# Performance work log

Measured on AMD Instinct MI355X. Metric: run time of the kernel, lower is better.

Reference implementation:

```python
import jax, jax.numpy as jnp
import numpy as np

DECAY = 0.9      # decay_rate l
LR = 0.5         # fast-weight learning_rate e
STEP = 3         # inner-loop iterations
EPS = 1e-3       # keras LayerNormalization default epsilon

B, D_IN, U = 128, 256, 512


def setup_inputs() -> dict:
    key = jax.random.key(0)
    ks = jax.random.split(key, 6)
    return {
        "inputs": jax.random.normal(ks[0], (B, D_IN), dtype=jnp.float32),
        "prev_state": jax.random.normal(ks[1], (B, U), dtype=jnp.float32),
        "A": jax.random.normal(ks[2], (B, U, U), dtype=jnp.float32) * 0.01,
        "C": jax.random.normal(ks[3], (D_IN, U), dtype=jnp.float32) * (1.0 / np.sqrt(D_IN)),
        # original: glorot-identity init scaled by 0.05; randomized here, same math
        "W_h": jax.random.normal(ks[4], (U, U), dtype=jnp.float32) * 0.05,
        "bias": jax.random.normal(ks[5], (U,), dtype=jnp.float32) * 0.01,
        "gamma": jnp.ones((U,), dtype=jnp.float32),
        "beta": jnp.zeros((U,), dtype=jnp.float32),
    }


def _layer_norm(x, gamma, beta):
    m = jnp.mean(x, axis=-1, keepdims=True)
    v = jnp.var(x, axis=-1, keepdims=True)
    return (x - m) * jax.lax.rsqrt(v + EPS) * gamma + beta


def reference(inputs, prev_state, A, C, W_h, bias, gamma, beta):
    # slow path: h = act(prev @ W_h + x @ C + b)   -> [B, U]
    pre = prev_state @ W_h + inputs @ C
    h = jnp.tanh(pre + bias)
    # fast-weight update: A' = l*A + e * outer(h, h)  -> [B, U, U]
    A_new = DECAY * A + LR * jnp.einsum("bi,bj->bij", h, h)
    # inner loop: h_s = LN(act(prelim + h_s @ A'))  with h_s: [B, 1, U]
    prelim = pre[:, None, :]          # no bias / no activation, matching source
    h_s = h[:, None, :]
    for _ in range(STEP):
        h_s = jnp.tanh(prelim + jnp.einsum("bku,buv->bkv", h_s, A_new))
        h_s = _layer_norm(h_s, gamma, beta)
    out = h_s[:, 0, :]                # [B, U]; also the new recurrent state
    return out, A_new
```

## Files before the change

### kernel.cpp

```cpp
#include <hip/hip_runtime.h>
#include <math.h>

#define UDIM 512
#define DIN  256
#define BATCH 128
#define EPSV 1e-3f

#define NRSEG 8
#define RPB   64
#define HALFR 32

typedef float f4 __attribute__((ext_vector_type(4)));

__global__ __launch_bounds__(256) void k_pre(
    const float* __restrict__ inputs, const float* __restrict__ prev,
    const float* __restrict__ C, const float* __restrict__ Wh,
    const float* __restrict__ bias, float* __restrict__ pre, float* __restrict__ h)
{
    const int b = blockIdx.x >> 1;
    const int v = ((blockIdx.x & 1) << 8) + threadIdx.x;

    __shared__ float sprev[UDIM];
    __shared__ float sinp[DIN];
    for (int i = threadIdx.x; i < UDIM; i += 256) sprev[i] = prev[b * UDIM + i];
    sinp[threadIdx.x] = inputs[b * DIN + threadIdx.x];
    __syncthreads();

    float acc = 0.f;
#pragma unroll 8
    for (int u = 0; u < UDIM; ++u) acc = fmaf(sprev[u], Wh[u * UDIM + v], acc);
#pragma unroll 8
    for (int i = 0; i < DIN; ++i)  acc = fmaf(sinp[i], C[i * UDIM + v], acc);

    pre[b * UDIM + v] = acc;
    h[b * UDIM + v]   = tanhf(acc + bias[v]);
}

__global__ __launch_bounds__(256) void k_mv0(
    const float* __restrict__ A, const float* __restrict__ h,
    float* __restrict__ Anew, float* __restrict__ ypart)
{
    const int bc   = blockIdx.x;
    const int b    = bc >> 3;
    const int rs   = bc & 7;
    const int t    = threadIdx.x;
    const int vg   = t & 127;
    const int col  = vg << 2;
    const int half = t >> 7;

    __shared__ __align__(16) float sh[UDIM];
    __shared__ __align__(16) float spart[2][UDIM];

    sh[t]       = h[(size_t)b * UDIM + t];
    sh[t + 256] = h[(size_t)b * UDIM + t + 256];
    __syncthreads();

    const f4 hv4 = *(const f4*)(sh + col);
    const int row0 = rs * RPB + half * HALFR;
    const float* __restrict__ Ab  = A    + ((size_t)b * UDIM + row0) * UDIM + col;
    float*       __restrict__ Anb = Anew + ((size_t)b * UDIM + row0) * UDIM + col;

    f4 acc = {0.f, 0.f, 0.f, 0.f};
#pragma unroll 8
    for (int k = 0; k < HALFR; ++k) {
        const f4 a4 = __builtin_nontemporal_load((const f4*)(Ab + (size_t)k * UDIM));
        const float hu = sh[row0 + k];
        const float s = 0.5f * hu;
        f4 an;
        an.x = fmaf(s, hv4.x, 0.9f * a4.x);
        an.y = fmaf(s, hv4.y, 0.9f * a4.y);
        an.z = fmaf(s, hv4.z, 0.9f * a4.z);
        an.w = fmaf(s, hv4.w, 0.9f * a4.w);
        *(f4*)(Anb + (size_t)k * UDIM) = an;
        acc.x = fmaf(hu, an.x, acc.x);
        acc.y = fmaf(hu, an.y, acc.y);
        acc.z = fmaf(hu, an.z, acc.z);
        acc.w = fmaf(hu, an.w, acc.w);
    }
    *(f4*)(&spart[half][col]) = acc;
    __syncthreads();

    {
        const float y0 = spart[0][t]       + spart[1][t];
        const float y1 = spart[0][t + 256] + spart[1][t + 256];
        ypart[(size_t)bc * UDIM + t]       = y0;
        ypart[(size_t)bc * UDIM + t + 256] = y1;
    }
}

__global__ __launch_bounds__(256) void k_mv(
    const float* __restrict__ An, const float* __restrict__ pre,
    const float* __restrict__ ypin, const float* __restrict__ gamma,
    const float* __restrict__ beta, float* __restrict__ ypout)
{
    const int bc   = blockIdx.x;
    const int b    = bc >> 3;
    const int rs   = bc & 7;
    const int t    = threadIdx.x;
    const int lane = t & 63;
    const int wave = t >> 6;
    const int vg   = t & 127;
    const int col  = vg << 2;
    const int half = t >> 7;

    __shared__ __align__(16) float sx[UDIM];
    __shared__ float shs[UDIM];
    __shared__ __align__(16) float spart[2][UDIM];
    __shared__ float sred[8];
    __shared__ float sbc[2];

    {
        float y0 = 0.f, y1 = 0.f;
#pragma unroll
        for (int s = 0; s < NRSEG; ++s) {
            y0 += ypin[((size_t)b * NRSEG + s) * UDIM + t];
            y1 += ypin[((size_t)b * NRSEG + s) * UDIM + t + 256];
        }
        const float hs0 = tanhf(pre[(size_t)b * UDIM + t] + y0);
        const float hs1 = tanhf(pre[(size_t)b * UDIM + t + 256] + y1);
        shs[t] = hs0; shs[t + 256] = hs1;
        float s1 = hs0 + hs1, s2 = hs0 * hs0 + hs1 * hs1;
#pragma unroll
        for (int off = 32; off; off >>= 1) {
            s1 += __shfl_xor(s1, off, 64);
            s2 += __shfl_xor(s2, off, 64);
        }
        if (lane == 0) { sred[wave] = s1; sred[4 + wave] = s2; }
    }
    __syncthreads();
    if (t == 0) {
        float m = sred[0] + sred[1] + sred[2] + sred[3];
        float q = sred[4] + sred[5] + sred[6] + sred[7];
        m *= (1.f / UDIM);
        q = q * (1.f / UDIM) - m * m;
        sbc[0] = m;
        sbc[1] = rsqrtf(q + EPSV);
    }
    __syncthreads();
    {
        const float m = sbc[0], r = sbc[1];
        sx[t]       = (shs[t]       - m) * r * gamma[t]       + beta[t];
        sx[t + 256] = (shs[t + 256] - m) * r * gamma[t + 256] + beta[t + 256];
    }
    __syncthreads();

    const int row0 = rs * RPB + half * HALFR;
    const float* __restrict__ Ab = An + ((size_t)b * UDIM + row0) * UDIM + col;

    f4 acc = {0.f, 0.f, 0.f, 0.f};
#pragma unroll 8
    for (int k = 0; k < HALFR; ++k) {
        const f4 a4 = *(const f4*)(Ab + (size_t)k * UDIM);
        const float xu = sx[row0 + k];
        acc.x = fmaf(xu, a4.x, acc.x);
        acc.y = fmaf(xu, a4.y, acc.y);
        acc.z = fmaf(xu, a4.z, acc.z);
        acc.w = fmaf(xu, a4.w, acc.w);
    }
    *(f4*)(&spart[half][col]) = acc;
    __syncthreads();

    {
        const float y0 = spart[0][t]       + spart[1][t];
        const float y1 = spart[0][t + 256] + spart[1][t + 256];
        ypout[(size_t)bc * UDIM + t]       = y0;
        ypout[(size_t)bc * UDIM + t + 256] = y1;
    }
}

__global__ __launch_bounds__(512) void k_fin(
    const float* __restrict__ pre, const float* __restrict__ ypin,
    const float* __restrict__ gamma, const float* __restrict__ beta,
    float* __restrict__ out)
{
    const int b    = blockIdx.x;
    const int t    = threadIdx.x;
    const int lane = t & 63;
    const int wave = t >> 6;

    __shared__ float sred[16];
    __shared__ float sbc[2];

    float y = 0.f;
#pragma unroll
    for (int s = 0; s < NRSEG; ++s) y += ypin[((size_t)b * NRSEG + s) * UDIM + t];
    const float hs = tanhf(pre[(size_t)b * UDIM + t] + y);

    float s1 = hs, s2 = hs * hs;
#pragma unroll
    for (int off = 32; off; off >>= 1) {
        s1 += __shfl_xor(s1, off, 64);
        s2 += __shfl_xor(s2, off, 64);
    }
    if (lane == 0) { sred[wave] = s1; sred[8 + wave] = s2; }
    __syncthreads();
    if (t == 0) {
        float m = 0.f, q = 0.f;
#pragma unroll
        for (int i = 0; i < 8; ++i) { m += sred[i]; q += sred[8 + i]; }
        m *= (1.f / UDIM);
        q = q * (1.f / UDIM) - m * m;
        sbc[0] = m;
        sbc[1] = rsqrtf(q + EPSV);
    }
    __syncthreads();
    out[(size_t)b * UDIM + t] = (hs - sbc[0]) * sbc[1] * gamma[t] + beta[t];
}

extern "C" void kernel_launch(void* const* d_in, const int* in_sizes, int n_in,
                              void* d_out, int out_size, void* d_ws, size_t ws_size,
                              hipStream_t stream) {
    const float* inputs = (const float*)d_in[0];
    const float* prev   = (const float*)d_in[1];
    const float* A      = (const float*)d_in[2];
    const float* C      = (const float*)d_in[3];
    const float* Wh     = (const float*)d_in[4];
    const float* bias   = (const float*)d_in[5];
    const float* gamma  = (const float*)d_in[6];
    const float* beta   = (const float*)d_in[7];

    float* out  = (float*)d_out;
    float* Anew = out + (size_t)BATCH * UDIM;

    float* pre  = (float*)d_ws;
    float* h    = pre  + (size_t)BATCH * UDIM;
    float* ypA  = h    + (size_t)BATCH * UDIM;
    float* ypB  = ypA  + (size_t)BATCH * NRSEG * UDIM;

    k_pre<<<BATCH * 2, 256, 0, stream>>>(inputs, prev, C, Wh, bias, pre, h);
    k_mv0<<<BATCH * NRSEG, 256, 0, stream>>>(A, h, Anew, ypA);
    k_mv <<<BATCH * NRSEG, 256, 0, stream>>>(Anew, pre, ypA, gamma, beta, ypB);
    k_mv <<<BATCH * NRSEG, 256, 0, stream>>>(Anew, pre, ypB, gamma, beta, ypA);
    k_fin<<<BATCH, 512, 0, stream>>>(pre, ypA, gamma, beta, out);
}
```

Before: 132.7 us.

## Use rank-1 identity to read original A and split Anew writes across passes

Rewrites x·A' as 0.9·(x·A) + 0.5·(x·h)·h, so every mat-vec pass reads the original A and adds a cheap dot-product correction instead of reading the freshly written Anew. The first pass now only reads A. The Anew write is split so each of the two later passes writes half the rows, using nontemporal stores. The aim is to spread and overlap the write traffic and avoid a write-then-read dependency, at the cost of extra dot-product reductions and small workspace buffers.

```diff
diff --git a/kernel.cpp b/kernel.cpp
--- a/kernel.cpp
+++ b/kernel.cpp
@@ -36,62 +36,9 @@
     h[b * UDIM + v]   = tanhf(acc + bias[v]);
 }
 
-__global__ __launch_bounds__(256) void k_mv0(
+__global__ __launch_bounds__(256) void k_mv0ro(
     const float* __restrict__ A, const float* __restrict__ h,
-    float* __restrict__ Anew, float* __restrict__ ypart)
-{
-    const int bc   = blockIdx.x;
-    const int b    = bc >> 3;
-    const int rs   = bc & 7;
-    const int t    = threadIdx.x;
-    const int vg   = t & 127;
-    const int col  = vg << 2;
-    const int half = t >> 7;
-
-    __shared__ __align__(16) float sh[UDIM];
-    __shared__ __align__(16) float spart[2][UDIM];
-
-    sh[t]       = h[(size_t)b * UDIM + t];
-    sh[t + 256] = h[(size_t)b * UDIM + t + 256];
-    __syncthreads();
-
-    const f4 hv4 = *(const f4*)(sh + col);
-    const int row0 = rs * RPB + half * HALFR;
-    const float* __restrict__ Ab  = A    + ((size_t)b * UDIM + row0) * UDIM + col;
-    float*       __restrict__ Anb = Anew + ((size_t)b * UDIM + row0) * UDIM + col;
-
-    f4 acc = {0.f, 0.f, 0.f, 0.f};
-#pragma unroll 8
-    for (int k = 0; k < HALFR; ++k) {
-        const f4 a4 = __builtin_nontemporal_load((const f4*)(Ab + (size_t)k * UDIM));
-        const float hu = sh[row0 + k];
-        const float s = 0.5f * hu;
-        f4 an;
-        an.x = fmaf(s, hv4.x, 0.9f * a4.x);
-        an.y = fmaf(s, hv4.y, 0.9f * a4.y);
-        an.z = fmaf(s, hv4.z, 0.9f * a4.z);
-        an.w = fmaf(s, hv4.w, 0.9f * a4.w);
-        *(f4*)(Anb + (size_t)k * UDIM) = an;
-        acc.x = fmaf(hu, an.x, acc.x);
-        acc.y = fmaf(hu, an.y, acc.y);
-        acc.z = fmaf(hu, an.z, acc.z);
-        acc.w = fmaf(hu, an.w, acc.w);
-    }
-    *(f4*)(&spart[half][col]) = acc;
-    __syncthreads();
-
-    {
-        const float y0 = spart[0][t]       + spart[1][t];
-        const float y1 = spart[0][t + 256] + spart[1][t + 256];
-        ypart[(size_t)bc * UDIM + t]       = y0;
-        ypart[(size_t)bc * UDIM + t + 256] = y1;
-    }
-}
-
-__global__ __launch_bounds__(256) void k_mv(
-    const float* __restrict__ An, const float* __restrict__ pre,
-    const float* __restrict__ ypin, const float* __restrict__ gamma,
-    const float* __restrict__ beta, float* __restrict__ ypout)
+    float* __restrict__ ypart, float* __restrict__ dotout)
 {
     const int bc   = blockIdx.x;
     const int b    = bc >> 3;
@@ -103,11 +50,72 @@
     const int col  = vg << 2;
     const int half = t >> 7;
 
+    __shared__ __align__(16) float sh[UDIM];
+    __shared__ __align__(16) float spart[2][UDIM];
+    __shared__ float sred[4];
+
+    sh[t]       = h[(size_t)b * UDIM + t];
+    sh[t + 256] = h[(size_t)b * UDIM + t + 256];
+    __syncthreads();
+
+    float dp = sh[t] * sh[t] + sh[t + 256] * sh[t + 256];
+#pragma unroll
+    for (int off = 32; off; off >>= 1) dp += __shfl_xor(dp, off, 64);
+    if (lane == 0) sred[wave] = dp;
+
+    const int row0 = rs * RPB + half * HALFR;
+    const float* __restrict__ Ab = A + ((size_t)b * UDIM + row0) * UDIM + col;
+
+    f4 acc = {0.f, 0.f, 0.f, 0.f};
+#pragma unroll 8
+    for (int k = 0; k < HALFR; ++k) {
+        const f4 a4 = *(const f4*)(Ab + (size_t)k * UDIM);
+        const float hu = sh[row0 + k];
+        acc.x = fmaf(hu, a4.x, acc.x);
+        acc.y = fmaf(hu, a4.y, acc.y);
+        acc.z = fmaf(hu, a4.z, acc.z);
+        acc.w = fmaf(hu, a4.w, acc.w);
+    }
+    *(f4*)(&spart[half][col]) = acc;
+    __syncthreads();
+
+    {
+        const float y0 = spart[0][t]       + spart[1][t];
+        const float y1 = spart[0][t + 256] + spart[1][t + 256];
+        ypart[(size_t)bc * UDIM + t]       = y0;
+        ypart[(size_t)bc * UDIM + t + 256] = y1;
+    }
+    if (rs == 0 && t == 0)
+        dotout[b] = sred[0] + sred[1] + sred[2] + sred[3];
+}
+
+__global__ __launch_bounds__(256) void k_mv(
+    const float* __restrict__ A, float* __restrict__ Anew,
+    const float* __restrict__ pre, const float* __restrict__ h,
+    const float* __restrict__ ypin, const float* __restrict__ dotin,
+    const float* __restrict__ gamma, const float* __restrict__ beta,
+    float* __restrict__ ypout, float* __restrict__ dotout, const int wh)
+{
+    const int bc   = blockIdx.x;
+    const int b    = bc >> 3;
+    const int rs   = bc & 7;
+    const int t    = threadIdx.x;
+    const int lane = t & 63;
+    const int wave = t >> 6;
+    const int vg   = t & 127;
+    const int col  = vg << 2;
+    const int half = t >> 7;
+
+    __shared__ __align__(16) float sh[UDIM];
     __shared__ __align__(16) float sx[UDIM];
     __shared__ float shs[UDIM];
     __shared__ __align__(16) float spart[2][UDIM];
     __shared__ float sred[8];
+    __shared__ float sred2[4];
     __shared__ float sbc[2];
+
+    sh[t]       = h[(size_t)b * UDIM + t];
+    sh[t + 256] = h[(size_t)b * UDIM + t + 256];
 
     {
         float y0 = 0.f, y1 = 0.f;
@@ -116,6 +124,9 @@
             y0 += ypin[((size_t)b * NRSEG + s) * UDIM + t];
             y1 += ypin[((size_t)b * NRSEG + s) * UDIM + t + 256];
         }
+        const float d = 0.5f * dotin[b];
+        y0 = fmaf(0.9f, y0, d * sh[t]);
+        y1 = fmaf(0.9f, y1, d * sh[t + 256]);
         const float hs0 = tanhf(pre[(size_t)b * UDIM + t] + y0);
         const float hs1 = tanhf(pre[(size_t)b * UDIM + t + 256] + y1);
         shs[t] = hs0; shs[t + 256] = hs1;
@@ -144,18 +155,46 @@
     }
     __syncthreads();
 
+    {
+        float dp = sx[t] * sh[t] + sx[t + 256] * sh[t + 256];
+#pragma unroll
+        for (int off = 32; off; off >>= 1) dp += __shfl_xor(dp, off, 64);
+        if (lane == 0) sred2[wave] = dp;
+    }
+
     const int row0 = rs * RPB + half * HALFR;
-    const float* __restrict__ Ab = An + ((size_t)b * UDIM + row0) * UDIM + col;
+    const float* __restrict__ Ab  = A    + ((size_t)b * UDIM + row0) * UDIM + col;
+    float*       __restrict__ Anb = Anew + ((size_t)b * UDIM + row0) * UDIM + col;
+    const f4 hv4 = *(const f4*)(sh + col);
 
     f4 acc = {0.f, 0.f, 0.f, 0.f};
-#pragma unroll 8
-    for (int k = 0; k < HALFR; ++k) {
-        const f4 a4 = *(const f4*)(Ab + (size_t)k * UDIM);
-        const float xu = sx[row0 + k];
-        acc.x = fmaf(xu, a4.x, acc.x);
-        acc.y = fmaf(xu, a4.y, acc.y);
-        acc.z = fmaf(xu, a4.z, acc.z);
-        acc.w = fmaf(xu, a4.w, acc.w);
+    if (half == wh) {
+#pragma unroll 8
+        for (int k = 0; k < HALFR; ++k) {
+            const f4 a4 = *(const f4*)(Ab + (size_t)k * UDIM);
+            const float xu = sx[row0 + k];
+            const float s  = 0.5f * sh[row0 + k];
+            f4 an;
+            an.x = fmaf(s, hv4.x, 0.9f * a4.x);
+            an.y = fmaf(s, hv4.y, 0.9f * a4.y);
+            an.z = fmaf(s, hv4.z, 0.9f * a4.z);
+            an.w = fmaf(s, hv4.w, 0.9f * a4.w);
+            __builtin_nontemporal_store(an, (f4*)(Anb + (size_t)k * UDIM));
+            acc.x = fmaf(xu, a4.x, acc.x);
+            acc.y = fmaf(xu, a4.y, acc.y);
+            acc.z = fmaf(xu, a4.z, acc.z);
+            acc.w = fmaf(xu, a4.w, acc.w);
+        }
+    } else {
+#pragma unroll 8
+        for (int k = 0; k < HALFR; ++k) {
+            const f4 a4 = *(const f4*)(Ab + (size_t)k * UDIM);
+            const float xu = sx[row0 + k];
+            acc.x = fmaf(xu, a4.x, acc.x);
+            acc.y = fmaf(xu, a4.y, acc.y);
+            acc.z = fmaf(xu, a4.z, acc.z);
+            acc.w = fmaf(xu, a4.w, acc.w);
+        }
     }
     *(f4*)(&spart[half][col]) = acc;
     __syncthreads();
@@ -166,10 +205,13 @@
         ypout[(size_t)bc * UDIM + t]       = y0;
         ypout[(size_t)bc * UDIM + t + 256] = y1;
     }
+    if (rs == 0 && t == 0)
+        dotout[b] = sred2[0] + sred2[1] + sred2[2] + sred2[3];
 }
 
 __global__ __launch_bounds__(512) void k_fin(
-    const float* __restrict__ pre, const float* __restrict__ ypin,
+    const float* __restrict__ pre, const float* __restrict__ h,
+    const float* __restrict__ ypin, const float* __restrict__ dotin,
     const float* __restrict__ gamma, const float* __restrict__ beta,
     float* __restrict__ out)
 {
@@ -184,6 +226,7 @@
     float y = 0.f;
 #pragma unroll
     for (int s = 0; s < NRSEG; ++s) y += ypin[((size_t)b * NRSEG + s) * UDIM + t];
+    y = fmaf(0.9f, y, 0.5f * dotin[b] * h[(size_t)b * UDIM + t]);
     const float hs = tanhf(pre[(size_t)b * UDIM + t] + y);
 
     float s1 = hs, s2 = hs * hs;
@@ -226,10 +269,15 @@
     float* h    = pre  + (size_t)BATCH * UDIM;
     float* ypA  = h    + (size_t)BATCH * UDIM;
     float* ypB  = ypA  + (size_t)BATCH * NRSEG * UDIM;
-
-    k_pre<<<BATCH * 2, 256, 0, stream>>>(inputs, prev, C, Wh, bias, pre, h);
-    k_mv0<<<BATCH * NRSEG, 256, 0, stream>>>(A, h, Anew, ypA);
-    k_mv <<<BATCH * NRSEG, 256, 0, stream>>>(Anew, pre, ypA, gamma, beta, ypB);
-    k_mv <<<BATCH * NRSEG, 256, 0, stream>>>(Anew, pre, ypB, gamma, beta, ypA);
-    k_fin<<<BATCH, 512, 0, stream>>>(pre, ypA, gamma, beta, out);
-}
+    float* dotH = ypB  + (size_t)BATCH * NRSEG * UDIM;
+    float* dot1 = dotH + BATCH;
+    float* dot2 = dot1 + BATCH;
+
+    k_pre  <<<BATCH * 2, 256, 0, stream>>>(inputs, prev, C, Wh, bias, pre, h);
+    k_mv0ro<<<BATCH * NRSEG, 256, 0, stream>>>(A, h, ypA, dotH);
+    k_mv   <<<BATCH * NRSEG, 256, 0, stream>>>(A, Anew, pre, h, ypA, dotH,
+                                               gamma, beta, ypB, dot1, 0);
+    k_mv   <<<BATCH * NRSEG, 256, 0, stream>>>(A, Anew, pre, h, ypB, dot1,
+                                               gamma, beta, ypA, dot2, 1);
+    k_fin  <<<BATCH, 512, 0, stream>>>(pre, h, ypA, dot2, gamma, beta, out);
+}
```

Measured after the change: 131.1 us. About the same (-1.2%).

## Split batch into two groups so Anew stays cache-resident across matvec passes

Applied to the files above, without the earlier changes.

The batch is processed in two halves of 64. Each half runs the A-update pass and then both inner matvec passes before the next half starts, so the 64 MB Anew slice for a half can be reused from the large last-level cache instead of being read back from HBM. Blocks grow to 512 threads with four 16-row quarters per slab. The nontemporal load hint on A is removed. The cost is twice as many kernel launches and smaller grids per launch, which may leave the device underfilled.

```diff
diff --git a/kernel.cpp b/kernel.cpp
--- a/kernel.cpp
+++ b/kernel.cpp
@@ -6,9 +6,10 @@
 #define BATCH 128
 #define EPSV 1e-3f
 
-#define NRSEG 8
+#define GRP   64
+#define NSLAB 8
 #define RPB   64
-#define HALFR 32
+#define QR    16
 
 typedef float f4 __attribute__((ext_vector_type(4)));
 
@@ -36,34 +37,33 @@
     h[b * UDIM + v]   = tanhf(acc + bias[v]);
 }
 
-__global__ __launch_bounds__(256) void k_mv0(
+__global__ __launch_bounds__(512) void k_mv0(
     const float* __restrict__ A, const float* __restrict__ h,
-    float* __restrict__ Anew, float* __restrict__ ypart)
-{
-    const int bc   = blockIdx.x;
-    const int b    = bc >> 3;
-    const int rs   = bc & 7;
-    const int t    = threadIdx.x;
-    const int vg   = t & 127;
-    const int col  = vg << 2;
-    const int half = t >> 7;
+    float* __restrict__ Anew, float* __restrict__ ypart, const int bofs)
+{
+    const int bc  = blockIdx.x;
+    const int b   = bofs + (bc >> 3);
+    const int rs  = bc & 7;
+    const int t   = threadIdx.x;
+    const int vg  = t & 127;
+    const int col = vg << 2;
+    const int qtr = t >> 7;
 
     __shared__ __align__(16) float sh[UDIM];
-    __shared__ __align__(16) float spart[2][UDIM];
-
-    sh[t]       = h[(size_t)b * UDIM + t];
-    sh[t + 256] = h[(size_t)b * UDIM + t + 256];
+    __shared__ __align__(16) float spart[4][UDIM];
+
+    sh[t] = h[(size_t)b * UDIM + t];
     __syncthreads();
 
     const f4 hv4 = *(const f4*)(sh + col);
-    const int row0 = rs * RPB + half * HALFR;
+    const int row0 = rs * RPB + qtr * QR;
     const float* __restrict__ Ab  = A    + ((size_t)b * UDIM + row0) * UDIM + col;
     float*       __restrict__ Anb = Anew + ((size_t)b * UDIM + row0) * UDIM + col;
 
     f4 acc = {0.f, 0.f, 0.f, 0.f};
 #pragma unroll 8
-    for (int k = 0; k < HALFR; ++k) {
-        const f4 a4 = __builtin_nontemporal_load((const f4*)(Ab + (size_t)k * UDIM));
+    for (int k = 0; k < QR; ++k) {
+        const f4 a4 = *(const f4*)(Ab + (size_t)k * UDIM);
         const float hu = sh[row0 + k];
         const float s = 0.5f * hu;
         f4 an;
@@ -77,79 +77,68 @@
         acc.z = fmaf(hu, an.z, acc.z);
         acc.w = fmaf(hu, an.w, acc.w);
     }
-    *(f4*)(&spart[half][col]) = acc;
-    __syncthreads();
-
-    {
-        const float y0 = spart[0][t]       + spart[1][t];
-        const float y1 = spart[0][t + 256] + spart[1][t + 256];
-        ypart[(size_t)bc * UDIM + t]       = y0;
-        ypart[(size_t)bc * UDIM + t + 256] = y1;
-    }
-}
-
-__global__ __launch_bounds__(256) void k_mv(
+    *(f4*)(&spart[qtr][col]) = acc;
+    __syncthreads();
+
+    ypart[((size_t)b * NSLAB + rs) * UDIM + t] =
+        spart[0][t] + spart[1][t] + spart[2][t] + spart[3][t];
+}
+
+__global__ __launch_bounds__(512) void k_mv(
     const float* __restrict__ An, const float* __restrict__ pre,
     const float* __restrict__ ypin, const float* __restrict__ gamma,
-    const float* __restrict__ beta, float* __restrict__ ypout)
+    const float* __restrict__ beta, float* __restrict__ ypout, const int bofs)
 {
     const int bc   = blockIdx.x;
-    const int b    = bc >> 3;
+    const int b    = bofs + (bc >> 3);
     const int rs   = bc & 7;
     const int t    = threadIdx.x;
     const int lane = t & 63;
     const int wave = t >> 6;
     const int vg   = t & 127;
     const int col  = vg << 2;
-    const int half = t >> 7;
+    const int qtr  = t >> 7;
 
     __shared__ __align__(16) float sx[UDIM];
-    __shared__ float shs[UDIM];
-    __shared__ __align__(16) float spart[2][UDIM];
-    __shared__ float sred[8];
+    __shared__ __align__(16) float spart[4][UDIM];
+    __shared__ float sred[16];
     __shared__ float sbc[2];
 
+    float hs;
     {
-        float y0 = 0.f, y1 = 0.f;
-#pragma unroll
-        for (int s = 0; s < NRSEG; ++s) {
-            y0 += ypin[((size_t)b * NRSEG + s) * UDIM + t];
-            y1 += ypin[((size_t)b * NRSEG + s) * UDIM + t + 256];
-        }
-        const float hs0 = tanhf(pre[(size_t)b * UDIM + t] + y0);
-        const float hs1 = tanhf(pre[(size_t)b * UDIM + t + 256] + y1);
-        shs[t] = hs0; shs[t + 256] = hs1;
-        float s1 = hs0 + hs1, s2 = hs0 * hs0 + hs1 * hs1;
+        float y = 0.f;
+#pragma unroll
+        for (int s = 0; s < NSLAB; ++s)
+            y += ypin[((size_t)b * NSLAB + s) * UDIM + t];
+        hs = tanhf(pre[(size_t)b * UDIM + t] + y);
+        float s1 = hs, s2 = hs * hs;
 #pragma unroll
         for (int off = 32; off; off >>= 1) {
             s1 += __shfl_xor(s1, off, 64);
             s2 += __shfl_xor(s2, off, 64);
         }
-        if (lane == 0) { sred[wave] = s1; sred[4 + wave] = s2; }
+        if (lane == 0) { sred[wave] = s1; sred[8 + wave] = s2; }
     }
     __syncthreads();
     if (t == 0) {
-        float m = sred[0] + sred[1] + sred[2] + sred[3];
-        float q = sred[4] + sred[5] + sred[6] + sred[7];
+        float m = 0.f, q = 0.f;
+#pragma unroll
+        for (int i = 0; i < 8; ++i) { m += sred[i]; q += sred[8 + i]; }
         m *= (1.f / UDIM);
         q = q * (1.f / UDIM) - m * m;
         sbc[0] = m;
         sbc[1] = rsqrtf(q + EPSV);
     }
     __syncthreads();
-    {
-        const float m = sbc[0], r = sbc[1];
-        sx[t]       = (shs[t]       - m) * r * gamma[t]       + beta[t];
-        sx[t + 256] = (shs[t + 256] - m) * r * gamma[t + 256] + beta[t + 256];
-    }
-    __syncthreads();
-
-    const int row0 = rs * RPB + half * HALFR;
+    sx[t] = (hs - sbc[0]) * sbc[1] * gamma[t] + beta[t];
+    __syncthreads();
+
+    const int row0 = rs * RPB + qtr * QR;
     const float* __restrict__ Ab = An + ((size_t)b * UDIM + row0) * UDIM + col;
 
     f4 acc = {0.f, 0.f, 0.f, 0.f};
 #pragma unroll 8
-    for (int k = 0; k < HALFR; ++k) {
+    for (int k = 0; k < QR; ++k) {
         const f4 a4 = *(const f4*)(Ab + (size_t)k * UDIM);
         const float xu = sx[row0 + k];
         acc.x = fmaf(xu, a4.x, acc.x);
@@ -157,15 +146,11 @@
         acc.z = fmaf(xu, a4.z, acc.z);
         acc.w = fmaf(xu, a4.w, acc.w);
     }
-    *(f4*)(&spart[half][col]) = acc;
-    __syncthreads();
-
-    {
-        const float y0 = spart[0][t]       + spart[1][t];
-        const float y1 = spart[0][t + 256] + spart[1][t + 256];
-        ypout[(size_t)bc * UDIM + t]       = y0;
-        ypout[(size_t)bc * UDIM + t + 256] = y1;
-    }
+    *(f4*)(&spart[qtr][col]) = acc;
+    __syncthreads();
+
+    ypout[((size_t)b * NSLAB + rs) * UDIM + t] =
+        spart[0][t] + spart[1][t] + spart[2][t] + spart[3][t];
 }
 
 __global__ __launch_bounds__(512) void k_fin(
@@ -183,7 +168,7 @@
 
     float y = 0.f;
 #pragma unroll
-    for (int s = 0; s < NRSEG; ++s) y += ypin[((size_t)b * NRSEG + s) * UDIM + t];
+    for (int s = 0; s < NSLAB; ++s) y += ypin[((size_t)b * NSLAB + s) * UDIM + t];
     const float hs = tanhf(pre[(size_t)b * UDIM + t] + y);
 
     float s1 = hs, s2 = hs * hs;
@@ -225,11 +210,17 @@
     float* pre  = (float*)d_ws;
     float* h    = pre  + (size_t)BATCH * UDIM;
     float* ypA  = h    + (size_t)BATCH * UDIM;
-    float* ypB  = ypA  + (size_t)BATCH * NRSEG * UDIM;
+    float* ypB  = ypA  + (size_t)BATCH * NSLAB * UDIM;
 
     k_pre<<<BATCH * 2, 256, 0, stream>>>(inputs, prev, C, Wh, bias, pre, h);
-    k_mv0<<<BATCH * NRSEG, 256, 0, stream>>>(A, h, Anew, ypA);
-    k_mv <<<BATCH * NRSEG, 256, 0, stream>>>(Anew, pre, ypA, gamma, beta, ypB);
-    k_mv <<<BATCH * NRSEG, 256, 0, stream>>>(Anew, pre, ypB, gamma, beta, ypA);
+
+    k_mv0<<<GRP * NSLAB, 512, 0, stream>>>(A, h, Anew, ypA, 0);
+    k_mv <<<GRP * NSLAB, 512, 0, stream>>>(Anew, pre, ypA, gamma, beta, ypB, 0);
+    k_mv <<<GRP * NSLAB, 512, 0, stream>>>(Anew, pre, ypB, gamma, beta, ypA, 0);
+
+    k_mv0<<<GRP * NSLAB, 512, 0, stream>>>(A, h, Anew, ypA, GRP);
+    k_mv <<<GRP * NSLAB, 512, 0, stream>>>(Anew, pre, ypA, gamma, beta, ypB, GRP);
+    k_mv <<<GRP * NSLAB, 512, 0, stream>>>(Anew, pre, ypB, gamma, beta, ypA, GRP);
+
     k_fin<<<BATCH, 512, 0, stream>>>(pre, ypA, gamma, beta, out);
 }
```

Measured after the change: 144.4 us. 8.8% more time.
